# Kernel tuning notes

Measured on AMD Instinct MI355X. Metric: run time of the kernel, lower is better.

Reference implementation:

```python
import jax, jax.numpy as jnp
import numpy as np

N_NODES = 100000
N_EDGES = 1200000
NFEAT, NHID, NCLASS = 64, 256, 40
DROP_RATE = 0.5
ORDER = 8


def setup_inputs() -> dict:
    key = jax.random.key(0)
    k = jax.random.split(key, 6)
    x = jax.random.normal(k[0], (N_NODES, NFEAT), dtype=jnp.float32)
    edge_index = jax.random.randint(k[1], (2, N_EDGES), 0, N_NODES, dtype=jnp.int64)
    stdv1 = 1.0 / np.sqrt(NHID)
    stdv2 = 1.0 / np.sqrt(NCLASS)
    W1 = jax.random.normal(k[2], (NFEAT, NHID), dtype=jnp.float32) * stdv1
    b1 = jax.random.normal(k[3], (NHID,), dtype=jnp.float32) * stdv1
    W2 = jax.random.normal(k[4], (NHID, NCLASS), dtype=jnp.float32) * stdv2
    b2 = jax.random.normal(k[5], (NCLASS,), dtype=jnp.float32) * stdv2
    return {"x": x, "edge_index": edge_index, "W1": W1, "b1": b1, "W2": W2, "b2": b2}


def _norm_adj(edge_index, n):
    # A + I, then D^{-1/2} (A+I) D^{-1/2}  (GCN symmetric normalization)
    loops = jnp.arange(n, dtype=edge_index.dtype)
    row = jnp.concatenate([edge_index[0], loops])
    col = jnp.concatenate([edge_index[1], loops])
    ones = jnp.ones(row.shape[0], dtype=jnp.float32)
    deg = jax.ops.segment_sum(ones, row, num_segments=n)  # row sums (self-loops guarantee deg>=1)
    d_inv_sqrt = 1.0 / jnp.sqrt(deg)
    ew = d_inv_sqrt[row] * d_inv_sqrt[col]  # [E+N] edge weights
    return row, col, ew


def reference(x, edge_index, W1, b1, W2, b2):
    n = x.shape[0]
    row, col, ew = _norm_adj(edge_index, n)

    def spmm(h):  # out[row] += ew * h[col]
        return jax.ops.segment_sum(ew[:, None] * h[col], row, num_segments=n)

    # eval-mode input scaling (training=False branch of GRAND.forward)
    h = x * (1.0 - DROP_RATE)
    y = h
    for _ in range(ORDER):
        h = spmm(h)
        y = y + h
    y = y / (ORDER + 1.0)

    # MLP in eval mode: dropouts are no-ops, use_bn=False
    hid = jax.nn.relu(y @ W1 + b1)
    return hid @ W2 + b2
```

## Files before the change

### kernel.cpp

```cpp
#include <hip/hip_runtime.h>

#define NN 100000
#define NE 1200000
#define NF 64
#define NH 256
#define NC 40
#define ORDER_C 8
#define SC 1024
#define BINB 2048
#define BCAP 165000

typedef __attribute__((ext_vector_type(8))) short short8;
typedef __attribute__((ext_vector_type(4))) float f32x4;

__device__ __forceinline__ unsigned bf16r(float x) {
    unsigned u = __float_as_uint(x);
    return (u + 0x7FFFu + ((u >> 16) & 1u)) >> 16;
}
__device__ __forceinline__ unsigned packbf(float lo, float hi) {
    return bf16r(lo) | (bf16r(hi) << 16);
}
__device__ __forceinline__ float bflo(unsigned u) { return __uint_as_float(u << 16); }
__device__ __forceinline__ float bfhi(unsigned u) { return __uint_as_float(u & 0xFFFF0000u); }


static __global__ __launch_bounds__(256) void k_bin(const int* __restrict__ rows,
                                                    const int* __restrict__ cols,
                                                    int* __restrict__ cnt,
                                                    int* __restrict__ bcnt,
                                                    int2* __restrict__ bbuf, int E)
{
    __shared__ int rbuf[BINB];
    __shared__ unsigned short lofs[BINB];
    __shared__ int hist[8], basew[8];
    int t = threadIdx.x;
    int e0 = blockIdx.x * BINB;
    int m = E - e0; if (m > BINB) m = BINB;
    if (t < 8) hist[t] = 0;
    __syncthreads();
    for (int i = t; i < m; i += 256) {
        int r = rows[e0 + i];
        rbuf[i] = r;
        atomicAdd(&cnt[r], 1);
        int b = r / 12500;
        lofs[i] = (unsigned short)atomicAdd(&hist[b], 1);
    }
    __syncthreads();
    if (t < 8) basew[t] = atomicAdd(&bcnt[t], hist[t]);
    __syncthreads();
    for (int i = t; i < m; i += 256) {
        int r = rbuf[i];
        int b = r / 12500;
        bbuf[(size_t)b * BCAP + basew[b] + lofs[i]] = make_int2(r, cols[e0 + i]);
    }
}


static __global__ __launch_bounds__(256) void k_bsum(const int* __restrict__ cnt,
                                                     int* __restrict__ bsum, int n)
{
    __shared__ int red[256];
    int t = threadIdx.x;
    int idx = blockIdx.x * SC + t * 4;
    int s = 0;
    if (idx + 3 < n) {
        int4 q = *(const int4*)&cnt[idx];
        s = q.x + q.y + q.z + q.w;
    } else {
        for (int j = 0; j < 4; ++j) if (idx + j < n) s += cnt[idx + j];
    }
    red[t] = s;
    __syncthreads();
    for (int off = 128; off > 0; off >>= 1) {
        if (t < off) red[t] += red[t + off];
        __syncthreads();
    }
    if (t == 0) bsum[blockIdx.x] = red[0];
}

static __global__ __launch_bounds__(128) void k_scanb(const int* __restrict__ bsum,
                                                      int* __restrict__ boff,
                                                      int* __restrict__ rp, int nb, int n)
{
    __shared__ int red[128];
    int t = threadIdx.x;
    int v = (t < nb) ? bsum[t] : 0;
    red[t] = v;
    __syncthreads();
    for (int off = 1; off < 128; off <<= 1) {
        int x = (t >= off) ? red[t - off] : 0;
        __syncthreads();
        red[t] += x;
        __syncthreads();
    }
    if (t < nb) boff[t] = (t == 0) ? 0 : red[t - 1];
    if (t == 0) rp[n] = red[127];
}

static __global__ __launch_bounds__(256) void k_scan3(const int* __restrict__ cnt,
                                                      const int* __restrict__ boff,
                                                      int* __restrict__ rp,
                                                      float2* __restrict__ drd, int n)
{
    __shared__ int red[256];
    int t = threadIdx.x;
    int idx = blockIdx.x * SC + t * 4;
    int v[4] = {0, 0, 0, 0};
    if (idx + 3 < n) {
        int4 q = *(const int4*)&cnt[idx];
        v[0] = q.x; v[1] = q.y; v[2] = q.z; v[3] = q.w;
    } else {
        for (int j = 0; j < 4; ++j) if (idx + j < n) v[j] = cnt[idx + j];
    }
    red[t] = v[0] + v[1] + v[2] + v[3];
    __syncthreads();
    for (int off = 1; off < 256; off <<= 1) {
        int x = (t >= off) ? red[t - off] : 0;
        __syncthreads();
        red[t] += x;
        __syncthreads();
    }
    int run = ((t == 0) ? 0 : red[t - 1]) + boff[blockIdx.x];
    #pragma unroll
    for (int j = 0; j < 4; ++j) {
        if (idx + j < n) {
            rp[idx + j] = run;
            float d1 = rsqrtf((float)(v[j] + 1));
            drd[idx + j] = make_float2(d1, (float)(v[j] + 1) * d1);
            run += v[j];
        }
    }
}


static __global__ __launch_bounds__(256) void k_scat2(const int2* __restrict__ bbuf,
                                                      const int* __restrict__ bcnt,
                                                      int* __restrict__ fillpos,
                                                      int* __restrict__ ccol)
{
    int grp = blockIdx.x & 7;
    int m = bcnt[grp];
    const int2* src = bbuf + (size_t)grp * BCAP;
    int stride = (gridDim.x >> 3) * 256;
    for (int i = (blockIdx.x >> 3) * 256 + threadIdx.x; i < m; i += stride) {
        int2 rc = src[i];
        int pos = atomicAdd(&fillpos[rc.x], 1);
        ccol[pos] = rc.y;
    }
}


static __global__ __launch_bounds__(256) void k_pack(const float* __restrict__ W1,
                                                     const float* __restrict__ W2,
                                                     unsigned short* __restrict__ w1f,
                                                     unsigned short* __restrict__ w2f)
{
    int t = blockIdx.x * 256 + threadIdx.x;
    if (t < 2048) {
        int lane = t & 63;
        int g = lane >> 4, col = (lane & 15) + ((t >> 6) & 15) * 16;
        int s = t >> 10;
        unsigned short* p = w1f + (size_t)t * 8;
        #pragma unroll
        for (int e = 0; e < 8; ++e) {
            int k = 32 * s + 8 * g + e;
            p[e] = (unsigned short)bf16r(W1[k * NH + col]);
        }
    } else if (t < 2048 + 1536) {
        int u = t - 2048;
        int lane = u & 63;
        int tile = u >> 6;
        int nt = tile % 3, s = tile / 3;
        int g = lane >> 4, col = (lane & 15) + nt * 16;
        unsigned short* p = w2f + (size_t)u * 8;
        #pragma unroll
        for (int e = 0; e < 8; ++e) {
            int k = 32 * s + 8 * g + e;
            p[e] = (col < NC) ? (unsigned short)bf16r(W2[k * NC + col]) : 0;
        }
    }
}


static __global__ __launch_bounds__(256) void k_init(const float4* __restrict__ x4,
                                                     float4* __restrict__ y4,
                                                     uint4* __restrict__ gb,
                                                     const float2* __restrict__ drd,
                                                     int nchunk)
{
    int i = blockIdx.x * 256 + threadIdx.x;
    if (i >= nchunk) return;
    float d1 = drd[i >> 3].x;
    float4 a = x4[i * 2], b = x4[i * 2 + 1];
    a.x *= 0.5f; a.y *= 0.5f; a.z *= 0.5f; a.w *= 0.5f;
    b.x *= 0.5f; b.y *= 0.5f; b.z *= 0.5f; b.w *= 0.5f;
    y4[i * 2] = a; y4[i * 2 + 1] = b;
    gb[i] = make_uint4(packbf(a.x * d1, a.y * d1), packbf(a.z * d1, a.w * d1),
                       packbf(b.x * d1, b.y * d1), packbf(b.z * d1, b.w * d1));
}


template<bool ACC>
static __global__ __launch_bounds__(256) void k_spmm(const uint2* __restrict__ gb,
                                                     uint2* __restrict__ go,
                                                     float4* __restrict__ y4,
                                                     const int* __restrict__ rp,
                                                     const int* __restrict__ ccol,
                                                     const float2* __restrict__ drd, int n)
{
    int wid  = (blockIdx.x * 256 + threadIdx.x) >> 6;
    int lane = threadIdx.x & 63;
    int row  = wid * 4 + (lane >> 4);
    int j    = lane & 15;
    if (row >= n) return;
    int s = rp[row], e = rp[row + 1];

    float a0 = 0.f, a1 = 0.f, a2 = 0.f, a3 = 0.f;
    float b0 = 0.f, b1 = 0.f, b2 = 0.f, b3 = 0.f;
    int i = s;
    for (; i + 7 < e; i += 8) {
        int c0 = ccol[i],     c1 = ccol[i + 1], c2 = ccol[i + 2], c3 = ccol[i + 3];
        int c4 = ccol[i + 4], c5 = ccol[i + 5], c6 = ccol[i + 6], c7 = ccol[i + 7];
        uint2 h0 = gb[(size_t)c0 * 16 + j];
        uint2 h1 = gb[(size_t)c1 * 16 + j];
        uint2 h2 = gb[(size_t)c2 * 16 + j];
        uint2 h3 = gb[(size_t)c3 * 16 + j];
        uint2 h4 = gb[(size_t)c4 * 16 + j];
        uint2 h5 = gb[(size_t)c5 * 16 + j];
        uint2 h6 = gb[(size_t)c6 * 16 + j];
        uint2 h7 = gb[(size_t)c7 * 16 + j];
        a0 += bflo(h0.x); a1 += bfhi(h0.x); a2 += bflo(h0.y); a3 += bfhi(h0.y);
        b0 += bflo(h1.x); b1 += bfhi(h1.x); b2 += bflo(h1.y); b3 += bfhi(h1.y);
        a0 += bflo(h2.x); a1 += bfhi(h2.x); a2 += bflo(h2.y); a3 += bfhi(h2.y);
        b0 += bflo(h3.x); b1 += bfhi(h3.x); b2 += bflo(h3.y); b3 += bfhi(h3.y);
        a0 += bflo(h4.x); a1 += bfhi(h4.x); a2 += bflo(h4.y); a3 += bfhi(h4.y);
        b0 += bflo(h5.x); b1 += bfhi(h5.x); b2 += bflo(h5.y); b3 += bfhi(h5.y);
        a0 += bflo(h6.x); a1 += bfhi(h6.x); a2 += bflo(h6.y); a3 += bfhi(h6.y);
        b0 += bflo(h7.x); b1 += bfhi(h7.x); b2 += bflo(h7.y); b3 += bfhi(h7.y);
    }
    for (; i + 3 < e; i += 4) {
        int c0 = ccol[i], c1 = ccol[i + 1], c2 = ccol[i + 2], c3 = ccol[i + 3];
        uint2 h0 = gb[(size_t)c0 * 16 + j];
        uint2 h1 = gb[(size_t)c1 * 16 + j];
        uint2 h2 = gb[(size_t)c2 * 16 + j];
        uint2 h3 = gb[(size_t)c3 * 16 + j];
        a0 += bflo(h0.x); a1 += bfhi(h0.x); a2 += bflo(h0.y); a3 += bfhi(h0.y);
        b0 += bflo(h1.x); b1 += bfhi(h1.x); b2 += bflo(h1.y); b3 += bfhi(h1.y);
        a0 += bflo(h2.x); a1 += bfhi(h2.x); a2 += bflo(h2.y); a3 += bfhi(h2.y);
        b0 += bflo(h3.x); b1 += bfhi(h3.x); b2 += bflo(h3.y); b3 += bfhi(h3.y);
    }
    for (; i < e; ++i) {
        uint2 h = gb[(size_t)ccol[i] * 16 + j];
        a0 += bflo(h.x); a1 += bfhi(h.x); a2 += bflo(h.y); a3 += bfhi(h.y);
    }

    float2 dr = drd[row];
    uint2 gs = gb[(size_t)row * 16 + j];
    float g0 = bflo(gs.x), g1 = bfhi(gs.x), g2 = bflo(gs.y), g3 = bfhi(gs.y);
    float s0 = (a0 + b0) + g0;
    float s1 = (a1 + b1) + g1;
    float s2 = (a2 + b2) + g2;
    float s3 = (a3 + b3) + g3;
    float h0 = dr.x * s0, h1 = dr.x * s1, h2 = dr.x * s2, h3 = dr.x * s3;
    go[(size_t)row * 16 + j] = make_uint2(packbf(dr.x * h0, dr.x * h1),
                                          packbf(dr.x * h2, dr.x * h3));
    if (ACC) {
        float4 yv = y4[(size_t)row * 16 + j];
        yv.x += fmaf(g0, dr.y, h0);
        yv.y += fmaf(g1, dr.y, h1);
        yv.z += fmaf(g2, dr.y, h2);
        yv.w += fmaf(g3, dr.y, h3);
        y4[(size_t)row * 16 + j] = yv;
    }
}


#define YSTR 72
#define HSTR 264

static __global__ __launch_bounds__(256) void k_mlp(const float4* __restrict__ y4,
                                                    const short8* __restrict__ w1f,
                                                    const short8* __restrict__ w2f,
                                                    const float* __restrict__ b1,
                                                    const float* __restrict__ b2,
                                                    float* __restrict__ out, int n)
{
    __shared__ short lds[64 * HSTR];
    int t = threadIdx.x;
    int lane = t & 63;
    int w = t >> 6;
    int base = blockIdx.x * 64;
    const float S = 1.f / 9.f;

    {
        int r = t >> 2, q = t & 3;
        int row = base + r;
        unsigned v[8];
        if (row < n) {
            const float4* yp = y4 + (size_t)row * 16 + q * 4;
            #pragma unroll
            for (int i = 0; i < 4; ++i) {
                float4 f = yp[i];
                v[i * 2]     = packbf(f.x * S, f.y * S);
                v[i * 2 + 1] = packbf(f.z * S, f.w * S);
            }
        } else {
            #pragma unroll
            for (int i = 0; i < 8; ++i) v[i] = 0;
        }
        uint4* dst = (uint4*)&lds[r * YSTR + q * 16];
        dst[0] = make_uint4(v[0], v[1], v[2], v[3]);
        dst[1] = make_uint4(v[4], v[5], v[6], v[7]);
    }
    __syncthreads();

    int m = lane & 15, g = lane >> 4;

    f32x4 acc[4][4];
    {
        short8 a[4][2];
        #pragma unroll
        for (int mt = 0; mt < 4; ++mt)
            #pragma unroll
            for (int s = 0; s < 2; ++s)
                a[mt][s] = *(const short8*)&lds[(mt * 16 + m) * YSTR + s * 32 + g * 8];
        #pragma unroll
        for (int nt4 = 0; nt4 < 4; ++nt4) {
            int nt = w * 4 + nt4;
            short8 b0  = w1f[nt * 64 + lane];
            short8 b1v = w1f[(16 + nt) * 64 + lane];
            float bias = b1[nt * 16 + m];
            #pragma unroll
            for (int mt = 0; mt < 4; ++mt) {
                f32x4 c = {bias, bias, bias, bias};
                c = __builtin_amdgcn_mfma_f32_16x16x32_bf16(a[mt][0], b0,  c, 0, 0, 0);
                c = __builtin_amdgcn_mfma_f32_16x16x32_bf16(a[mt][1], b1v, c, 0, 0, 0);
                acc[mt][nt4] = c;
            }
        }
    }
    __syncthreads();

    {
        #pragma unroll
        for (int mt = 0; mt < 4; ++mt)
            #pragma unroll
            for (int nt4 = 0; nt4 < 4; ++nt4) {
                int col = w * 64 + nt4 * 16 + m;
                #pragma unroll
                for (int r = 0; r < 4; ++r) {
                    float hv = fmaxf(acc[mt][nt4][r], 0.f);
                    lds[(mt * 16 + g * 4 + r) * HSTR + col] = (short)bf16r(hv);
                }
            }
    }
    __syncthreads();

    {
        short8 a2[8];
        #pragma unroll
        for (int s = 0; s < 8; ++s)
            a2[s] = *(const short8*)&lds[(w * 16 + m) * HSTR + s * 32 + g * 8];
        #pragma unroll
        for (int nt = 0; nt < 3; ++nt) {
            int col = nt * 16 + m;
            float bias = (col < NC) ? b2[col] : 0.f;
            f32x4 c = {bias, bias, bias, bias};
            #pragma unroll
            for (int s = 0; s < 8; ++s)
                c = __builtin_amdgcn_mfma_f32_16x16x32_bf16(a2[s], w2f[(s * 3 + nt) * 64 + lane], c, 0, 0, 0);
            if (col < NC) {
                #pragma unroll
                for (int r = 0; r < 4; ++r) {
                    int row = base + w * 16 + g * 4 + r;
                    if (row < n) out[(size_t)row * NC + col] = c[r];
                }
            }
        }
    }
}


extern "C" void kernel_launch(void* const* d_in, const int* in_sizes, int n_in,
                              void* d_out, int out_size, void* d_ws, size_t ws_size,
                              hipStream_t stream)
{
    const float* x  = (const float*)d_in[0];
    const int*   ei = (const int*)d_in[1];
    const float* W1 = (const float*)d_in[2];
    const float* b1 = (const float*)d_in[3];
    const float* W2 = (const float*)d_in[4];
    const float* b2 = (const float*)d_in[5];
    float* out = (float*)d_out;

    const int n = NN, E = NE;
    const int nb = (n + SC - 1) / SC;

    char* ws = (char*)d_ws;
    size_t off = 0;
    auto alloc = [&](size_t bytes) -> void* {
        void* p = ws + off;
        off = (off + bytes + 255) & ~(size_t)255;
        return p;
    };
    int*    cnt  = (int*)   alloc((size_t)n * 4);
    int*    fill = (int*)   alloc((size_t)n * 4);
    int*    rp   = (int*)   alloc((size_t)(n + 1) * 4);
    float2* drd  = (float2*)alloc((size_t)n * 8);
    int*    bsum = (int*)   alloc(128 * 4);
    int*    boff = (int*)   alloc(128 * 4);
    int*    bcnt = (int*)   alloc(8 * 4);
    int2*   bbuf = (int2*)  alloc((size_t)8 * BCAP * 8);
    int*    ccol = (int*)   alloc((size_t)E * 4);
    unsigned short* w1f = (unsigned short*)alloc(2048 * 8 * 2);
    unsigned short* w2f = (unsigned short*)alloc(1536 * 8 * 2);
    uint4* ha   = (uint4*)alloc((size_t)n * NF * 2);
    uint4* hbuf = (uint4*)alloc((size_t)n * NF * 2);
    float* y    = (float*)alloc((size_t)n * NF * 4);

    hipMemsetAsync(cnt, 0, (size_t)n * 4, stream);
    hipMemsetAsync(bcnt, 0, 8 * 4, stream);

    const int* rows = ei;
    const int* cols = ei + E;

    k_bin   <<<(E + BINB - 1) / BINB, 256, 0, stream>>>(rows, cols, cnt, bcnt, bbuf, E);
    k_bsum  <<<nb, 256, 0, stream>>>(cnt, bsum, n);
    k_scanb <<<1, 128, 0, stream>>>(bsum, boff, rp, nb, n);
    k_scan3 <<<nb, 256, 0, stream>>>(cnt, boff, rp, drd, n);
    hipMemcpyAsync(fill, rp, (size_t)n * 4, hipMemcpyDeviceToDevice, stream);
    k_scat2 <<<4096, 256, 0, stream>>>(bbuf, bcnt, fill, ccol);
    k_pack  <<<14, 256, 0, stream>>>(W1, W2, w1f, w2f);

    int nchunk = n * 8;
    k_init<<<(nchunk + 255) / 256, 256, 0, stream>>>((const float4*)x, (float4*)y,
                                                     ha, drd, nchunk);

    uint4* cur = ha;
    uint4* nxt = hbuf;
    int spmm_blocks = (n + 15) / 16;
    for (int it = 0; it < ORDER_C; ++it) {
        if (it & 1)
            k_spmm<true><<<spmm_blocks, 256, 0, stream>>>((const uint2*)cur, (uint2*)nxt,
                                                          (float4*)y, rp, ccol, drd, n);
        else
            k_spmm<false><<<spmm_blocks, 256, 0, stream>>>((const uint2*)cur, (uint2*)nxt,
                                                           (float4*)y, rp, ccol, drd, n);
        uint4* tswap = cur; cur = nxt; nxt = tswap;
    }

    k_mlp<<<(n + 63) / 64, 256, 0, stream>>>((const float4*)y, (const short8*)w1f,
                                             (const short8*)w2f, b1, b2, out, n);
}
```

Baseline: 403.1 us.

## Pad CSR rows to multiples of eight with a zero dummy node

Each row's neighbor list is padded to a multiple of 8 entries that point at an extra all-zero feature row (index n). The SpMM inner loop then uses only vectorized int4 index loads with no remainder loops. Degree counting moves out of the binning kernel into a separate pass over the binned rows, the bin buffer is split into separate row and column arrays, and the binning block size is halved. The cost is more edges to process, extra fill and count kernels, and larger buffers.

```diff
diff --git a/kernel.cpp b/kernel.cpp
--- a/kernel.cpp
+++ b/kernel.cpp
@@ -7,8 +7,9 @@
 #define NC 40
 #define ORDER_C 8
 #define SC 1024
-#define BINB 2048
+#define BINB 1024
 #define BCAP 165000
+#define CCAP (NE + 7 * NN)
 
 typedef __attribute__((ext_vector_type(8))) short short8;
 typedef __attribute__((ext_vector_type(4))) float f32x4;
@@ -26,9 +27,9 @@
 
 static __global__ __launch_bounds__(256) void k_bin(const int* __restrict__ rows,
                                                     const int* __restrict__ cols,
-                                                    int* __restrict__ cnt,
                                                     int* __restrict__ bcnt,
-                                                    int2* __restrict__ bbuf, int E)
+                                                    int* __restrict__ browb,
+                                                    int* __restrict__ bcolb, int E)
 {
     __shared__ int rbuf[BINB];
     __shared__ unsigned short lofs[BINB];
@@ -41,7 +42,6 @@
     for (int i = t; i < m; i += 256) {
         int r = rows[e0 + i];
         rbuf[i] = r;
-        atomicAdd(&cnt[r], 1);
         int b = r / 12500;
         lofs[i] = (unsigned short)atomicAdd(&hist[b], 1);
     }
@@ -51,8 +51,23 @@
     for (int i = t; i < m; i += 256) {
         int r = rbuf[i];
         int b = r / 12500;
-        bbuf[(size_t)b * BCAP + basew[b] + lofs[i]] = make_int2(r, cols[e0 + i]);
-    }
+        size_t pos = (size_t)b * BCAP + basew[b] + lofs[i];
+        browb[pos] = r;
+        bcolb[pos] = cols[e0 + i];
+    }
+}
+
+
+static __global__ __launch_bounds__(256) void k_cnt2(const int* __restrict__ browb,
+                                                     const int* __restrict__ bcnt,
+                                                     int* __restrict__ cnt)
+{
+    int grp = blockIdx.x & 7;
+    int m = bcnt[grp];
+    const int* src = browb + (size_t)grp * BCAP;
+    int stride = (gridDim.x >> 3) * 256;
+    for (int i = (blockIdx.x >> 3) * 256 + threadIdx.x; i < m; i += stride)
+        atomicAdd(&cnt[src[i]], 1);
 }
 
 
@@ -65,9 +80,9 @@
     int s = 0;
     if (idx + 3 < n) {
         int4 q = *(const int4*)&cnt[idx];
-        s = q.x + q.y + q.z + q.w;
+        s = ((q.x + 7) & ~7) + ((q.y + 7) & ~7) + ((q.z + 7) & ~7) + ((q.w + 7) & ~7);
     } else {
-        for (int j = 0; j < 4; ++j) if (idx + j < n) s += cnt[idx + j];
+        for (int j = 0; j < 4; ++j) if (idx + j < n) s += (cnt[idx + j] + 7) & ~7;
     }
     red[t] = s;
     __syncthreads();
@@ -112,7 +127,10 @@
     } else {
         for (int j = 0; j < 4; ++j) if (idx + j < n) v[j] = cnt[idx + j];
     }
-    red[t] = v[0] + v[1] + v[2] + v[3];
+    int p[4];
+    #pragma unroll
+    for (int j = 0; j < 4; ++j) p[j] = (v[j] + 7) & ~7;
+    red[t] = p[0] + p[1] + p[2] + p[3];
     __syncthreads();
     for (int off = 1; off < 256; off <<= 1) {
         int x = (t >= off) ? red[t - off] : 0;
@@ -127,25 +145,34 @@
             rp[idx + j] = run;
             float d1 = rsqrtf((float)(v[j] + 1));
             drd[idx + j] = make_float2(d1, (float)(v[j] + 1) * d1);
-            run += v[j];
-        }
-    }
-}
-
-
-static __global__ __launch_bounds__(256) void k_scat2(const int2* __restrict__ bbuf,
+            run += p[j];
+        }
+    }
+}
+
+
+static __global__ __launch_bounds__(256) void k_fillc(int4* __restrict__ ccol4, int cap4, int val)
+{
+    int i = blockIdx.x * 256 + threadIdx.x;
+    if (i < cap4) ccol4[i] = make_int4(val, val, val, val);
+}
+
+
+static __global__ __launch_bounds__(256) void k_scat2(const int* __restrict__ browb,
+                                                      const int* __restrict__ bcolb,
                                                       const int* __restrict__ bcnt,
                                                       int* __restrict__ fillpos,
                                                       int* __restrict__ ccol)
 {
     int grp = blockIdx.x & 7;
     int m = bcnt[grp];
-    const int2* src = bbuf + (size_t)grp * BCAP;
+    const int* srcr = browb + (size_t)grp * BCAP;
+    const int* srcc = bcolb + (size_t)grp * BCAP;
     int stride = (gridDim.x >> 3) * 256;
     for (int i = (blockIdx.x >> 3) * 256 + threadIdx.x; i < m; i += stride) {
-        int2 rc = src[i];
-        int pos = atomicAdd(&fillpos[rc.x], 1);
-        ccol[pos] = rc.y;
+        int r = srcr[i];
+        int pos = atomicAdd(&fillpos[r], 1);
+        ccol[pos] = srcc[i];
     }
 }
 
@@ -184,18 +211,25 @@
 
 static __global__ __launch_bounds__(256) void k_init(const float4* __restrict__ x4,
                                                      float4* __restrict__ y4,
-                                                     uint4* __restrict__ gb,
+                                                     uint4* __restrict__ ga,
+                                                     uint4* __restrict__ gbp,
                                                      const float2* __restrict__ drd,
                                                      int nchunk)
 {
     int i = blockIdx.x * 256 + threadIdx.x;
-    if (i >= nchunk) return;
+    if (i >= nchunk) {
+        if (i < nchunk + 8) {
+            uint4 z = make_uint4(0, 0, 0, 0);
+            ga[i] = z; gbp[i] = z;
+        }
+        return;
+    }
     float d1 = drd[i >> 3].x;
     float4 a = x4[i * 2], b = x4[i * 2 + 1];
     a.x *= 0.5f; a.y *= 0.5f; a.z *= 0.5f; a.w *= 0.5f;
     b.x *= 0.5f; b.y *= 0.5f; b.z *= 0.5f; b.w *= 0.5f;
     y4[i * 2] = a; y4[i * 2 + 1] = b;
-    gb[i] = make_uint4(packbf(a.x * d1, a.y * d1), packbf(a.z * d1, a.w * d1),
+    ga[i] = make_uint4(packbf(a.x * d1, a.y * d1), packbf(a.z * d1, a.w * d1),
                        packbf(b.x * d1, b.y * d1), packbf(b.z * d1, b.w * d1));
 }
 
@@ -217,18 +251,17 @@
 
     float a0 = 0.f, a1 = 0.f, a2 = 0.f, a3 = 0.f;
     float b0 = 0.f, b1 = 0.f, b2 = 0.f, b3 = 0.f;
-    int i = s;
-    for (; i + 7 < e; i += 8) {
-        int c0 = ccol[i],     c1 = ccol[i + 1], c2 = ccol[i + 2], c3 = ccol[i + 3];
-        int c4 = ccol[i + 4], c5 = ccol[i + 5], c6 = ccol[i + 6], c7 = ccol[i + 7];
-        uint2 h0 = gb[(size_t)c0 * 16 + j];
-        uint2 h1 = gb[(size_t)c1 * 16 + j];
-        uint2 h2 = gb[(size_t)c2 * 16 + j];
-        uint2 h3 = gb[(size_t)c3 * 16 + j];
-        uint2 h4 = gb[(size_t)c4 * 16 + j];
-        uint2 h5 = gb[(size_t)c5 * 16 + j];
-        uint2 h6 = gb[(size_t)c6 * 16 + j];
-        uint2 h7 = gb[(size_t)c7 * 16 + j];
+    for (int i = s; i < e; i += 8) {
+        int4 cA = *(const int4*)&ccol[i];
+        int4 cB = *(const int4*)&ccol[i + 4];
+        uint2 h0 = gb[(size_t)cA.x * 16 + j];
+        uint2 h1 = gb[(size_t)cA.y * 16 + j];
+        uint2 h2 = gb[(size_t)cA.z * 16 + j];
+        uint2 h3 = gb[(size_t)cA.w * 16 + j];
+        uint2 h4 = gb[(size_t)cB.x * 16 + j];
+        uint2 h5 = gb[(size_t)cB.y * 16 + j];
+        uint2 h6 = gb[(size_t)cB.z * 16 + j];
+        uint2 h7 = gb[(size_t)cB.w * 16 + j];
         a0 += bflo(h0.x); a1 += bfhi(h0.x); a2 += bflo(h0.y); a3 += bfhi(h0.y);
         b0 += bflo(h1.x); b1 += bfhi(h1.x); b2 += bflo(h1.y); b3 += bfhi(h1.y);
         a0 += bflo(h2.x); a1 += bfhi(h2.x); a2 += bflo(h2.y); a3 += bfhi(h2.y);
@@ -237,21 +270,6 @@
         b0 += bflo(h5.x); b1 += bfhi(h5.x); b2 += bflo(h5.y); b3 += bfhi(h5.y);
         a0 += bflo(h6.x); a1 += bfhi(h6.x); a2 += bflo(h6.y); a3 += bfhi(h6.y);
         b0 += bflo(h7.x); b1 += bfhi(h7.x); b2 += bflo(h7.y); b3 += bfhi(h7.y);
-    }
-    for (; i + 3 < e; i += 4) {
-        int c0 = ccol[i], c1 = ccol[i + 1], c2 = ccol[i + 2], c3 = ccol[i + 3];
-        uint2 h0 = gb[(size_t)c0 * 16 + j];
-        uint2 h1 = gb[(size_t)c1 * 16 + j];
-        uint2 h2 = gb[(size_t)c2 * 16 + j];
-        uint2 h3 = gb[(size_t)c3 * 16 + j];
-        a0 += bflo(h0.x); a1 += bfhi(h0.x); a2 += bflo(h0.y); a3 += bfhi(h0.y);
-        b0 += bflo(h1.x); b1 += bfhi(h1.x); b2 += bflo(h1.y); b3 += bfhi(h1.y);
-        a0 += bflo(h2.x); a1 += bfhi(h2.x); a2 += bflo(h2.y); a3 += bfhi(h2.y);
-        b0 += bflo(h3.x); b1 += bfhi(h3.x); b2 += bflo(h3.y); b3 += bfhi(h3.y);
-    }
-    for (; i < e; ++i) {
-        uint2 h = gb[(size_t)ccol[i] * 16 + j];
-        a0 += bflo(h.x); a1 += bfhi(h.x); a2 += bflo(h.y); a3 += bfhi(h.y);
     }
 
     float2 dr = drd[row];
@@ -403,19 +421,20 @@
         off = (off + bytes + 255) & ~(size_t)255;
         return p;
     };
-    int*    cnt  = (int*)   alloc((size_t)n * 4);
-    int*    fill = (int*)   alloc((size_t)n * 4);
-    int*    rp   = (int*)   alloc((size_t)(n + 1) * 4);
-    float2* drd  = (float2*)alloc((size_t)n * 8);
-    int*    bsum = (int*)   alloc(128 * 4);
-    int*    boff = (int*)   alloc(128 * 4);
-    int*    bcnt = (int*)   alloc(8 * 4);
-    int2*   bbuf = (int2*)  alloc((size_t)8 * BCAP * 8);
-    int*    ccol = (int*)   alloc((size_t)E * 4);
+    int*    cnt   = (int*)   alloc((size_t)n * 4);
+    int*    fill  = (int*)   alloc((size_t)n * 4);
+    int*    rp    = (int*)   alloc((size_t)(n + 1) * 4);
+    float2* drd   = (float2*)alloc((size_t)n * 8);
+    int*    bsum  = (int*)   alloc(128 * 4);
+    int*    boff  = (int*)   alloc(128 * 4);
+    int*    bcnt  = (int*)   alloc(8 * 4);
+    int*    browb = (int*)   alloc((size_t)8 * BCAP * 4);
+    int*    bcolb = (int*)   alloc((size_t)8 * BCAP * 4);
+    int*    ccol  = (int*)   alloc((size_t)CCAP * 4);
     unsigned short* w1f = (unsigned short*)alloc(2048 * 8 * 2);
     unsigned short* w2f = (unsigned short*)alloc(1536 * 8 * 2);
-    uint4* ha   = (uint4*)alloc((size_t)n * NF * 2);
-    uint4* hbuf = (uint4*)alloc((size_t)n * NF * 2);
+    uint4* ha   = (uint4*)alloc((size_t)(n + 1) * NF * 2);
+    uint4* hbuf = (uint4*)alloc((size_t)(n + 1) * NF * 2);
     float* y    = (float*)alloc((size_t)n * NF * 4);
 
     hipMemsetAsync(cnt, 0, (size_t)n * 4, stream);
@@ -424,17 +443,19 @@
     const int* rows = ei;
     const int* cols = ei + E;
 
-    k_bin   <<<(E + BINB - 1) / BINB, 256, 0, stream>>>(rows, cols, cnt, bcnt, bbuf, E);
+    k_bin   <<<(E + BINB - 1) / BINB, 256, 0, stream>>>(rows, cols, bcnt, browb, bcolb, E);
+    k_cnt2  <<<4096, 256, 0, stream>>>(browb, bcnt, cnt);
     k_bsum  <<<nb, 256, 0, stream>>>(cnt, bsum, n);
     k_scanb <<<1, 128, 0, stream>>>(bsum, boff, rp, nb, n);
     k_scan3 <<<nb, 256, 0, stream>>>(cnt, boff, rp, drd, n);
     hipMemcpyAsync(fill, rp, (size_t)n * 4, hipMemcpyDeviceToDevice, stream);
-    k_scat2 <<<4096, 256, 0, stream>>>(bbuf, bcnt, fill, ccol);
+    k_fillc <<<(CCAP / 4 + 255) / 256, 256, 0, stream>>>((int4*)ccol, CCAP / 4, n);
+    k_scat2 <<<4096, 256, 0, stream>>>(browb, bcolb, bcnt, fill, ccol);
     k_pack  <<<14, 256, 0, stream>>>(W1, W2, w1f, w2f);
 
     int nchunk = n * 8;
-    k_init<<<(nchunk + 255) / 256, 256, 0, stream>>>((const float4*)x, (float4*)y,
-                                                     ha, drd, nchunk);
+    k_init<<<(nchunk + 8 + 255) / 256, 256, 0, stream>>>((const float4*)x, (float4*)y,
+                                                         ha, hbuf, drd, nchunk);
 
     uint4* cur = ha;
     uint4* nxt = hbuf;
```

Result: no change. 405.9 us (+0.7%).
